# Optimization experiments

Hardware: AMD Instinct MI355X
Metric: run time of the kernel (lower is better)

Reference implementation:

```python
import jax, jax.numpy as jnp
import numpy as np

W_DIM, B_DIM, S = 8, 8, 900  # patches: [W, B, 1, 30, 30] -> seq_len 900


def setup_inputs() -> dict:
    key = jax.random.key(0)
    ks = jax.random.split(key, 8)
    radar = jax.random.normal(ks[0], (W_DIM, B_DIM, 1, 30, 30), jnp.float32)
    dmde = jax.random.normal(ks[1], (W_DIM, B_DIM, 1, 30, 30), jnp.float32)
    gumbel_u = jax.random.uniform(ks[2], (B_DIM * W_DIM, S, S), jnp.float32)
    # MHA with embed_dim=1 -> all projections are scalars (xavier-ish init)
    Wq = jax.random.normal(ks[3], (), jnp.float32)
    Wk = jax.random.normal(ks[4], (), jnp.float32)
    Wv = jax.random.normal(ks[5], (), jnp.float32)
    Wo = jax.random.normal(ks[6], (), jnp.float32)
    bq = jnp.zeros((), jnp.float32)
    bk = jnp.zeros((), jnp.float32)
    bv = jnp.zeros((), jnp.float32)
    bo = jnp.zeros((), jnp.float32)
    ln_gamma = jnp.ones((), jnp.float32)
    ln_beta = jnp.zeros((), jnp.float32)
    attn_residual_scale = jnp.asarray(1e-9, jnp.float32)
    return dict(radar_patches=radar, dmde_out_patches=dmde, gumbel_u=gumbel_u,
                Wq=Wq, bq=bq, Wk=Wk, bk=bk, Wv=Wv, bv=bv, Wo=Wo, bo=bo,
                ln_gamma=ln_gamma, ln_beta=ln_beta,
                attn_residual_scale=attn_residual_scale)


def reference(radar_patches, dmde_out_patches, gumbel_u, Wq, bq, Wk, bk, Wv, bv,
              Wo, bo, ln_gamma, ln_beta, attn_residual_scale):
    Wd, B = radar_patches.shape[0], radar_patches.shape[1]
    # [W,B,1,30,30] -> [B*W, S]
    radar = jnp.transpose(radar_patches, (1, 0, 2, 3, 4)).reshape(B * Wd, -1)
    mde = jnp.transpose(dmde_out_patches, (1, 0, 2, 3, 4)).reshape(B * Wd, -1)
    # --- cross attention, embed_dim = head_dim = 1 (scale = 1/sqrt(1) = 1) ---
    q = radar * Wq + bq
    k = mde * Wk + bk
    v = mde * Wv + bv
    attn = jax.nn.softmax(jnp.einsum('ni,nj->nij', q, k), axis=-1)  # [N,S,S]
    attended = jnp.einsum('nij,nj->ni', attn, v) * Wo + bo           # [N,S]
    # LayerNorm over last dim of size 1 (degenerate: output == ln_beta)
    x = (radar + attended)[..., None]                                # [N,S,1]
    mu = jnp.mean(x, axis=-1, keepdims=True)
    var = jnp.mean((x - mu) ** 2, axis=-1, keepdims=True)
    attended_out = (x - mu) / jnp.sqrt(var + 1e-5) * ln_gamma + ln_beta
    # --- hard gumbel attention gather/scatter, fully mask-vectorized ---
    valid = (radar != 0).astype(radar.dtype)                          # [N,S]
    noise = -jnp.log(-jnp.log(gumbel_u + 1e-8) + 1e-8)
    p = jax.nn.softmax(attn + noise, axis=-1)  # temperature = 1.0
    idx = jnp.argmax(p, axis=-1)                                      # [N,S]
    y_hard = jax.nn.one_hot(idx, p.shape[-1], dtype=p.dtype)
    y = jax.lax.stop_gradient(y_hard - p) + p                         # straight-through
    src = radar * valid   # invalid rows contribute nothing (matches per-row loop)
    out_seq = jnp.einsum('nts,nt->ns', y, src)[..., None]             # [N,S,1]
    combined = valid[..., None] * (out_seq != 0).astype(out_seq.dtype)
    out_seq = out_seq + combined * (attn_residual_scale * attended_out)
    # [N,S] -> [B,W,S] -> [B,1,S,W]
    out = out_seq[..., 0].reshape(B, Wd, -1).transpose(0, 2, 1)[:, None]
    return out
```

## Files before the change

kernel.cpp:

```cpp
#include <hip/hip_runtime.h>
#include <cfloat>

#define SS 900
#define WD 8
#define BD 8
#define NROWS 64
#define OUT_ELEMS (BD * SS * WD)
#define NQ 225
#define KPAD 904

__global__ __launch_bounds__(256) void rel_prep(
    const float* __restrict__ mde,
    const float* __restrict__ pWk, const float* __restrict__ pbk,
    float* __restrict__ kws,
    float* __restrict__ kext,
    float* __restrict__ out)
{
    const int tid = threadIdx.x;
    const int n   = blockIdx.x;

    for (int i = n * 256 + tid; i < OUT_ELEMS; i += 64 * 256) out[i] = 0.0f;

    const float wk = pWk[0], bk0 = pbk[0];
    const int b = n >> 3, w = n & 7;
    const float* __restrict__ mrow = mde + (size_t)(w * BD + b) * SS;

    float kmin = FLT_MAX, kmax = -FLT_MAX;
    #pragma unroll
    for (int j = 0; j < 4; j++) {
        int s = j * 256 + tid;
        if (s < SS) {
            float k = __fmaf_rn(mrow[s], wk, bk0);
            kws[(size_t)n * KPAD + s] = k;
            kmin = fminf(kmin, k);
            kmax = fmaxf(kmax, k);
        }
    }
    #pragma unroll
    for (int off = 1; off < 64; off <<= 1) {
        kmin = fminf(kmin, __shfl_xor(kmin, off, 64));
        kmax = fmaxf(kmax, __shfl_xor(kmax, off, 64));
    }
    __shared__ float s_min[4], s_max[4];
    if ((tid & 63) == 0) { s_min[tid >> 6] = kmin; s_max[tid >> 6] = kmax; }
    __syncthreads();
    if (tid == 0) {
        kext[2 * n]     = fminf(fminf(s_min[0], s_min[1]), fminf(s_min[2], s_min[3]));
        kext[2 * n + 1] = fmaxf(fmaxf(s_max[0], s_max[1]), fmaxf(s_max[2], s_max[3]));
    }
}

__global__ __launch_bounds__(256) void rel_main(
    const float* __restrict__ radar,
    const float* __restrict__ gumbel,
    const float* __restrict__ kws,
    const float* __restrict__ kext,
    const float* __restrict__ pWq, const float* __restrict__ pbq,
    float* __restrict__ out)
{
    const int tid    = threadIdx.x;
    const int wid    = tid >> 6;
    const int g      = (tid >> 4) & 3;
    const int lane16 = tid & 15;
    const int row    = blockIdx.x * 16 + wid * 4 + g;
    const int n      = row / SS;
    const int t      = row - n * SS;
    const int b      = n >> 3;
    const int w      = n & 7;

    const float4* __restrict__ g4 = (const float4*)(gumbel + (size_t)row * SS);
    const float4* __restrict__ k4 = (const float4*)(kws + (size_t)n * KPAD);
    const float*  __restrict__ krow = kws + (size_t)n * KPAD;

    const float r0 = radar[(size_t)(w * BD + b) * SS + t];
    const float q  = __fmaf_rn(r0, pWq[0], pbq[0]);
    const float kmin = kext[2 * n], kmax = kext[2 * n + 1];
    const float m = __fmul_rn(q, (q >= 0.0f) ? kmax : kmin);

    float4 U[15];
    float umax = -1.0f;
    float D = 0.0f;
    #pragma unroll
    for (int j = 0; j < 15; j++) {
        const int f = j * 16 + lane16;
        const bool valid = (j < 14) || (lane16 == 0);
        const int fc = valid ? f : 0;
        float4 u = g4[fc];
        float4 k = k4[fc];
        if (!valid) { u.x = u.y = u.z = u.w = -1.0f; }
        U[j] = u;
        umax = fmaxf(umax, fmaxf(fmaxf(u.x, u.y), fmaxf(u.z, u.w)));
        if (valid) {
            D += __expf(__fmaf_rn(q, k.x, -m)) + __expf(__fmaf_rn(q, k.y, -m))
               + __expf(__fmaf_rn(q, k.z, -m)) + __expf(__fmaf_rn(q, k.w, -m));
        }
    }
    #pragma unroll
    for (int off = 1; off < 16; off <<= 1) {
        umax = fmaxf(umax, __shfl_xor(umax, off, 16));
        D += __shfl_xor(D, off, 16);
    }

    float margin = __fmaf_rn(1.002f, 1.0f / D, 1e-6f);
    float w0    = -logf(umax + 1e-8f);
    float nzmax = -logf(w0 + 1e-8f);
    float T     = nzmax - margin;
    float wT    = expf(-T);
    float uthr  = expf(-(wT - 1e-8f)) - 1e-8f;
    uthr = uthr - fabsf(uthr) * 4e-6f - 1e-9f;

    float bestv = -FLT_MAX;
    int   besti = 0x7fffffff;
    #pragma unroll
    for (int j = 0; j < 15; j++) {
        float4 u = U[j];
        float m4 = fmaxf(fmaxf(u.x, u.y), fmaxf(u.z, u.w));
        if (__any(m4 >= uthr)) {
            const int s0 = (j * 16 + lane16) * 4;
            if (u.x >= uthr) {
                float l = __fmul_rn(q, krow[s0]);
                float nz = -logf(-logf(u.x + 1e-8f) + 1e-8f);
                float v = expf(l - m) / D + nz;
                if (v > bestv) { bestv = v; besti = s0; }
            }
            if (u.y >= uthr) {
                float l = __fmul_rn(q, krow[s0 + 1]);
                float nz = -logf(-logf(u.y + 1e-8f) + 1e-8f);
                float v = expf(l - m) / D + nz;
                if (v > bestv) { bestv = v; besti = s0 + 1; }
            }
            if (u.z >= uthr) {
                float l = __fmul_rn(q, krow[s0 + 2]);
                float nz = -logf(-logf(u.z + 1e-8f) + 1e-8f);
                float v = expf(l - m) / D + nz;
                if (v > bestv) { bestv = v; besti = s0 + 2; }
            }
            if (u.w >= uthr) {
                float l = __fmul_rn(q, krow[s0 + 3]);
                float nz = -logf(-logf(u.w + 1e-8f) + 1e-8f);
                float v = expf(l - m) / D + nz;
                if (v > bestv) { bestv = v; besti = s0 + 3; }
            }
        }
    }
    #pragma unroll
    for (int off = 1; off < 16; off <<= 1) {
        float ov = __shfl_xor(bestv, off, 16);
        int   oi = __shfl_xor(besti, off, 16);
        if (ov > bestv || (ov == bestv && oi < besti)) { bestv = ov; besti = oi; }
    }
    if (lane16 == 0)
        atomicAdd(&out[((size_t)b * SS + besti) * WD + w], r0);
}

__global__ __launch_bounds__(256) void rel_epilogue(
    const float* __restrict__ radar,
    const float* __restrict__ pScale,
    const float* __restrict__ pBeta,
    float* __restrict__ out)
{
    int i = blockIdx.x * 256 + threadIdx.x;
    if (i >= OUT_ELEMS) return;
    int w    = i & 7;
    int rest = i >> 3;
    int s    = rest % SS;
    int b    = rest / SS;
    float o = out[i];
    float r = radar[(size_t)(w * BD + b) * SS + s];
    float add = ((r != 0.0f) && (o != 0.0f)) ? (pScale[0] * pBeta[0]) : 0.0f;
    out[i] = o + add;
}

extern "C" void kernel_launch(void* const* d_in, const int* in_sizes, int n_in,
                              void* d_out, int out_size, void* d_ws, size_t ws_size,
                              hipStream_t stream) {
    const float* radar  = (const float*)d_in[0];
    const float* mde    = (const float*)d_in[1];
    const float* gumbel = (const float*)d_in[2];
    const float* Wq     = (const float*)d_in[3];
    const float* bq     = (const float*)d_in[4];
    const float* Wk     = (const float*)d_in[5];
    const float* bk     = (const float*)d_in[6];
    const float* beta   = (const float*)d_in[12];
    const float* scale  = (const float*)d_in[13];
    float* out = (float*)d_out;

    float* kws  = (float*)d_ws;
    float* kext = kws + (size_t)NROWS * KPAD;

    rel_prep<<<NROWS, 256, 0, stream>>>(mde, Wk, bk, kws, kext, out);
    rel_main<<<(NROWS * SS) / 16, 256, 0, stream>>>(radar, gumbel, kws, kext, Wq, bq, out);
    rel_epilogue<<<(OUT_ELEMS + 255) / 256, 256, 0, stream>>>(radar, scale, beta, out);
}
```

Before: 46.43 us.

## Fuse key prep into main kernel with per-block shared-memory keys

Removes the separate key-prep kernel and its global workspace. Each main block now recomputes its batch row's 900 scaled keys and their min/max into shared memory, and reads keys from LDS instead of global memory. Blocks are remapped so each covers 16 query rows of a single batch row, with a partial tail block. Output zeroing moves to a small standalone kernel. The trade-off is redundant key computation in every block (57 per batch row) and a block-wide sync, in exchange for dropping a dependent global round trip.

```diff
diff --git a/kernel.cpp b/kernel.cpp
--- a/kernel.cpp
+++ b/kernel.cpp
@@ -7,75 +7,67 @@
 #define NROWS 64
 #define OUT_ELEMS (BD * SS * WD)
 #define NQ 225
-#define KPAD 904
+#define ROWS_PER_BLK 16
+#define BLKS_PER_N 57
 
-__global__ __launch_bounds__(256) void rel_prep(
+__global__ __launch_bounds__(256) void rel_zero(float* __restrict__ out) {
+    int i = blockIdx.x * 256 + threadIdx.x;
+    if (i < OUT_ELEMS) out[i] = 0.0f;
+}
+
+__global__ __launch_bounds__(256) void rel_main(
+    const float* __restrict__ radar,
     const float* __restrict__ mde,
+    const float* __restrict__ gumbel,
+    const float* __restrict__ pWq, const float* __restrict__ pbq,
     const float* __restrict__ pWk, const float* __restrict__ pbk,
-    float* __restrict__ kws,
-    float* __restrict__ kext,
     float* __restrict__ out)
 {
-    const int tid = threadIdx.x;
-    const int n   = blockIdx.x;
+    const int tid   = threadIdx.x;
+    const int n     = blockIdx.x / BLKS_PER_N;
+    const int tbase = (blockIdx.x - n * BLKS_PER_N) * ROWS_PER_BLK;
+    const int b     = n >> 3;
+    const int w     = n & 7;
 
-    for (int i = n * 256 + tid; i < OUT_ELEMS; i += 64 * 256) out[i] = 0.0f;
+    __shared__ float4 ks4[NQ + 1];
+    __shared__ float  s_red[8];
 
     const float wk = pWk[0], bk0 = pbk[0];
-    const int b = n >> 3, w = n & 7;
-    const float* __restrict__ mrow = mde + (size_t)(w * BD + b) * SS;
-
     float kmin = FLT_MAX, kmax = -FLT_MAX;
-    #pragma unroll
-    for (int j = 0; j < 4; j++) {
-        int s = j * 256 + tid;
-        if (s < SS) {
-            float k = __fmaf_rn(mrow[s], wk, bk0);
-            kws[(size_t)n * KPAD + s] = k;
-            kmin = fminf(kmin, k);
-            kmax = fmaxf(kmax, k);
-        }
+    if (tid < NQ) {
+        const float4* __restrict__ m4 = (const float4*)(mde + (size_t)(w * BD + b) * SS);
+        float4 mq = m4[tid];
+        float4 k;
+        k.x = __fmaf_rn(mq.x, wk, bk0);
+        k.y = __fmaf_rn(mq.y, wk, bk0);
+        k.z = __fmaf_rn(mq.z, wk, bk0);
+        k.w = __fmaf_rn(mq.w, wk, bk0);
+        ks4[tid] = k;
+        kmin = fminf(fminf(k.x, k.y), fminf(k.z, k.w));
+        kmax = fmaxf(fmaxf(k.x, k.y), fmaxf(k.z, k.w));
     }
     #pragma unroll
     for (int off = 1; off < 64; off <<= 1) {
         kmin = fminf(kmin, __shfl_xor(kmin, off, 64));
         kmax = fmaxf(kmax, __shfl_xor(kmax, off, 64));
     }
-    __shared__ float s_min[4], s_max[4];
-    if ((tid & 63) == 0) { s_min[tid >> 6] = kmin; s_max[tid >> 6] = kmax; }
+    if ((tid & 63) == 0) { s_red[tid >> 6] = kmin; s_red[4 + (tid >> 6)] = kmax; }
     __syncthreads();
-    if (tid == 0) {
-        kext[2 * n]     = fminf(fminf(s_min[0], s_min[1]), fminf(s_min[2], s_min[3]));
-        kext[2 * n + 1] = fmaxf(fmaxf(s_max[0], s_max[1]), fmaxf(s_max[2], s_max[3]));
-    }
-}
+    kmin = fminf(fminf(s_red[0], s_red[1]), fminf(s_red[2], s_red[3]));
+    kmax = fmaxf(fmaxf(s_red[4], s_red[5]), fmaxf(s_red[6], s_red[7]));
 
-__global__ __launch_bounds__(256) void rel_main(
-    const float* __restrict__ radar,
-    const float* __restrict__ gumbel,
-    const float* __restrict__ kws,
-    const float* __restrict__ kext,
-    const float* __restrict__ pWq, const float* __restrict__ pbq,
-    float* __restrict__ out)
-{
-    const int tid    = threadIdx.x;
-    const int wid    = tid >> 6;
-    const int g      = (tid >> 4) & 3;
+    const int gg     = tid >> 4;
     const int lane16 = tid & 15;
-    const int row    = blockIdx.x * 16 + wid * 4 + g;
-    const int n      = row / SS;
-    const int t      = row - n * SS;
-    const int b      = n >> 3;
-    const int w      = n & 7;
-
-    const float4* __restrict__ g4 = (const float4*)(gumbel + (size_t)row * SS);
-    const float4* __restrict__ k4 = (const float4*)(kws + (size_t)n * KPAD);
-    const float*  __restrict__ krow = kws + (size_t)n * KPAD;
+    const int t      = tbase + gg;
+    if (t >= SS) return;
+    const int row = n * SS + t;
 
     const float r0 = radar[(size_t)(w * BD + b) * SS + t];
     const float q  = __fmaf_rn(r0, pWq[0], pbq[0]);
-    const float kmin = kext[2 * n], kmax = kext[2 * n + 1];
-    const float m = __fmul_rn(q, (q >= 0.0f) ? kmax : kmin);
+    const float m  = __fmul_rn(q, (q >= 0.0f) ? kmax : kmin);
+
+    const float4* __restrict__ g4 = (const float4*)(gumbel + (size_t)row * SS);
+    const float*  __restrict__ kf = (const float*)ks4;
 
     float4 U[15];
     float umax = -1.0f;
@@ -86,7 +78,7 @@
         const bool valid = (j < 14) || (lane16 == 0);
         const int fc = valid ? f : 0;
         float4 u = g4[fc];
-        float4 k = k4[fc];
+        float4 k = ks4[fc];
         if (!valid) { u.x = u.y = u.z = u.w = -1.0f; }
         U[j] = u;
         umax = fmaxf(umax, fmaxf(fmaxf(u.x, u.y), fmaxf(u.z, u.w)));
@@ -118,25 +110,25 @@
         if (__any(m4 >= uthr)) {
             const int s0 = (j * 16 + lane16) * 4;
             if (u.x >= uthr) {
-                float l = __fmul_rn(q, krow[s0]);
+                float l = __fmul_rn(q, kf[s0]);
                 float nz = -logf(-logf(u.x + 1e-8f) + 1e-8f);
                 float v = expf(l - m) / D + nz;
                 if (v > bestv) { bestv = v; besti = s0; }
             }
             if (u.y >= uthr) {
-                float l = __fmul_rn(q, krow[s0 + 1]);
+                float l = __fmul_rn(q, kf[s0 + 1]);
                 float nz = -logf(-logf(u.y + 1e-8f) + 1e-8f);
                 float v = expf(l - m) / D + nz;
                 if (v > bestv) { bestv = v; besti = s0 + 1; }
             }
             if (u.z >= uthr) {
-                float l = __fmul_rn(q, krow[s0 + 2]);
+                float l = __fmul_rn(q, kf[s0 + 2]);
                 float nz = -logf(-logf(u.z + 1e-8f) + 1e-8f);
                 float v = expf(l - m) / D + nz;
                 if (v > bestv) { bestv = v; besti = s0 + 2; }
             }
             if (u.w >= uthr) {
-                float l = __fmul_rn(q, krow[s0 + 3]);
+                float l = __fmul_rn(q, kf[s0 + 3]);
                 float nz = -logf(-logf(u.w + 1e-8f) + 1e-8f);
                 float v = expf(l - m) / D + nz;
                 if (v > bestv) { bestv = v; besti = s0 + 3; }
@@ -185,10 +177,8 @@
     const float* scale  = (const float*)d_in[13];
     float* out = (float*)d_out;
 
-    float* kws  = (float*)d_ws;
-    float* kext = kws + (size_t)NROWS * KPAD;
-
-    rel_prep<<<NROWS, 256, 0, stream>>>(mde, Wk, bk, kws, kext, out);
-    rel_main<<<(NROWS * SS) / 16, 256, 0, stream>>>(radar, gumbel, kws, kext, Wq, bq, out);
+    rel_zero<<<(OUT_ELEMS + 255) / 256, 256, 0, stream>>>(out);
+    rel_main<<<NROWS * BLKS_PER_N, 256, 0, stream>>>(radar, mde, gumbel,
+                                                     Wq, bq, Wk, bk, out);
     rel_epilogue<<<(OUT_ELEMS + 255) / 256, 256, 0, stream>>>(radar, scale, beta, out);
 }
```

Measured after the change: 45.04 us. 3.0% less time.
